# Kernel optimization log

Hardware: AMD Instinct MI355X
Metric: run time of the kernel (lower is better)

Reference implementation:

```python
import jax, jax.numpy as jnp
import numpy as np

N, E = 50000, 800000
IN, HID, HEADS, OUT = 128, 32, 8, 40
D1 = HID * HEADS  # 256


def setup_inputs() -> dict:
    key = jax.random.key(0)
    ks = jax.random.split(key, 24)

    def w(k, fin, fout):
        return (jax.random.normal(k, (fin, fout), jnp.float32) / np.sqrt(fin)).astype(jnp.float32)

    def b(k, fout):
        return (jax.random.normal(k, (fout,), jnp.float32) * 0.02).astype(jnp.float32)

    inp = {
        "x": jax.random.normal(ks[0], (N, IN), jnp.float32),
        "edge_index": jax.random.randint(ks[1], (2, E), 0, N, dtype=jnp.int64),
        # layer 1: TransformerConv(IN -> HID, heads=HEADS, concat=True, beta=True)
        "q1w": w(ks[2], IN, D1), "q1b": b(ks[3], D1),
        "k1w": w(ks[4], IN, D1), "k1b": b(ks[5], D1),
        "v1w": w(ks[6], IN, D1), "v1b": b(ks[7], D1),
        "s1w": w(ks[8], IN, D1), "s1b": b(ks[9], D1),
        "b1w": w(ks[10], 3 * D1, 1),
        # layer 2: TransformerConv(D1 -> OUT, heads=1, concat=False, beta=True)
        "q2w": w(ks[11], D1, OUT), "q2b": b(ks[12], OUT),
        "k2w": w(ks[13], D1, OUT), "k2b": b(ks[14], OUT),
        "v2w": w(ks[15], D1, OUT), "v2b": b(ks[16], OUT),
        "s2w": w(ks[17], D1, OUT), "s2b": b(ks[18], OUT),
        "b2w": w(ks[19], 3 * OUT, 1),
    }
    return inp


def _tconv(x, src, dst, qw, qb, kw, kb, vw, vb, sw, sb, bw, heads, ch, concat):
    """PyG TransformerConv (no edge_attr, root_weight=True, beta=True), eval mode."""
    n = x.shape[0]
    q = (x @ qw + qb).reshape(n, heads, ch)
    k = (x @ kw + kb).reshape(n, heads, ch)
    v = (x @ vw + vb).reshape(n, heads, ch)
    # per-edge attention logits: message flows src(j) -> dst(i)
    alpha = jnp.einsum("ehc,ehc->eh", q[dst], k[src]) / np.sqrt(ch)  # [E,H]
    # segment softmax over incoming edges of each dst node
    amax = jax.ops.segment_max(alpha, dst, num_segments=n)  # [N,H]
    a = jnp.exp(alpha - amax[dst])
    asum = jax.ops.segment_sum(a, dst, num_segments=n)  # [N,H]
    attn = a / asum[dst]  # [E,H]
    # scatter-aggregate weighted values
    out = jax.ops.segment_sum(v[src] * attn[:, :, None], dst, num_segments=n)  # [N,H,C]
    out = out.reshape(n, heads * ch) if concat else out.mean(axis=1)
    skip = x @ sw + sb
    beta = jax.nn.sigmoid(jnp.concatenate([out, skip, out - skip], axis=-1) @ bw)  # [N,1]
    return beta * skip + (1.0 - beta) * out


def reference(x, edge_index, q1w, q1b, k1w, k1b, v1w, v1b, s1w, s1b, b1w,
              q2w, q2b, k2w, k2b, v2w, v2b, s2w, s2b, b2w):
    src, dst = edge_index[0], edge_index[1]
    h = jax.nn.elu(_tconv(x, src, dst, q1w, q1b, k1w, k1b, v1w, v1b, s1w, s1b, b1w, HEADS, HID, True))
    return _tconv(h, src, dst, q2w, q2b, k2w, k2b, v2w, v2b, s2w, s2b, b2w, 1, OUT, False)
```

## Files before the change

### kernel.cpp

```cpp
#include <hip/hip_runtime.h>
#include <cstdint>
#include <cstddef>

#define N_NODES 50000
#define N_EDGES 800000
#define IN_F    128
#define HID     32
#define HEADS   8
#define OUT_F   40
#define D1      256
#define W1COLS  1024
#define W2COLS  160
#define CAP     64

#define GFILL_B   3125
#define G1_BX     391
#define G1_BY     8
#define G1_GEMM_B (G1_BX * G1_BY)
#define G1_TOTAL  (GFILL_B + G1_GEMM_B)

typedef unsigned short ushortT;
typedef unsigned char  ucharT;
typedef unsigned short ushortx8 __attribute__((ext_vector_type(8)));
typedef __bf16 bf16x8 __attribute__((ext_vector_type(8)));
typedef float floatx4 __attribute__((ext_vector_type(4)));
typedef float floatx2 __attribute__((ext_vector_type(2)));

__device__ inline ushortT f2bf(float f) {
    union { float f; unsigned int u; } c; c.f = f;
    unsigned int r = c.u + 0x7FFFu + ((c.u >> 16) & 1u);
    return (ushortT)(r >> 16);
}
__device__ inline float bf2f(ushortT h) {
    union { unsigned int u; float f; } c; c.u = ((unsigned int)h) << 16; return c.f;
}

#define PREP_Z_B     196
#define PREP_CONV_B  6250
#define PREP_W1_B    512
#define PREP_W2_B    160
#define PREP_TOTAL_B (PREP_Z_B + PREP_CONV_B + PREP_W1_B + PREP_W2_B)

__global__ __launch_bounds__(256) void k_prep(
        int* __restrict__ cursor,
        const float* __restrict__ x, ushortT* __restrict__ xb,
        const float* __restrict__ q1w, const float* __restrict__ k1w,
        const float* __restrict__ v1w, const float* __restrict__ s1w,
        const float* __restrict__ q1b, const float* __restrict__ k1b,
        const float* __restrict__ v1b, const float* __restrict__ s1b,
        ushortT* __restrict__ W1T, float* __restrict__ b1c,
        const float* __restrict__ q2w, const float* __restrict__ k2w,
        const float* __restrict__ v2w, const float* __restrict__ s2w,
        const float* __restrict__ q2b, const float* __restrict__ k2b,
        const float* __restrict__ v2b, const float* __restrict__ s2b,
        ushortT* __restrict__ W2T, float* __restrict__ b2c) {
    int b = blockIdx.x;
    int tid = threadIdx.x;
    if (b < PREP_Z_B) {
        int i = b * 256 + tid;
        if (i < N_NODES) cursor[i] = 0;
    } else if (b < PREP_Z_B + PREP_CONV_B) {
        int i = (b - PREP_Z_B) * 256 + tid;
        float4 v = reinterpret_cast<const float4*>(x)[i];
        ushort4 o;
        o.x = f2bf(v.x); o.y = f2bf(v.y); o.z = f2bf(v.z); o.w = f2bf(v.w);
        reinterpret_cast<ushort4*>(xb)[i] = o;
    } else if (b < PREP_Z_B + PREP_CONV_B + PREP_W1_B) {
        int t = (b - PREP_Z_B - PREP_CONV_B) * 256 + tid;
        int c = t / IN_F, k = t % IN_F;
        int sel = c >> 8, cc = c & 255;
        const float* w = sel == 0 ? q1w : sel == 1 ? k1w : sel == 2 ? v1w : s1w;
        W1T[(size_t)c * IN_F + k] = f2bf(w[(size_t)k * D1 + cc]);
        if (k == 0) {
            const float* bb = sel == 0 ? q1b : sel == 1 ? k1b : sel == 2 ? v1b : s1b;
            b1c[c] = bb[cc];
        }
    } else {
        int t = (b - PREP_Z_B - PREP_CONV_B - PREP_W1_B) * 256 + tid;
        int c = t / D1, k = t % D1;
        int sel = c / OUT_F, cc = c % OUT_F;
        const float* w = sel == 0 ? q2w : sel == 1 ? k2w : sel == 2 ? v2w : s2w;
        W2T[(size_t)c * D1 + k] = f2bf(w[(size_t)k * OUT_F + cc]);
        if (k == 0) {
            const float* bb = sel == 0 ? q2b : sel == 1 ? k2b : sel == 2 ? v2b : s2b;
            b2c[c] = bb[cc];
        }
    }
}

template<int MODE>
__global__ __launch_bounds__(256) void gemm_mfma_pack(
        const ushortT* __restrict__ A, const ushortT* __restrict__ BT,
        const float* __restrict__ bias, float* __restrict__ QSf,
        ushortT* __restrict__ QSh, ucharT* __restrict__ KV8,
        ushortT* __restrict__ K2V2,
        const int* __restrict__ ei, int* __restrict__ cursor, int* __restrict__ col,
        int M, int K, int Nn) {
    constexpr int TM = 128, TN = 128, TK = 32, LDP = 40;
    __shared__ ushortT smem[TM * LDP + TN * LDP];
    ushortT* As = smem;
    ushortT* Bs = smem + TM * LDP;
    int bx2, by2;
    if (MODE == 1) {
        int t = blockIdx.x;
        int idx;
        bool isFill;
        if (t < 2 * GFILL_B) { isFill = !(t & 1); idx = t >> 1; }
        else                 { isFill = false;    idx = t - GFILL_B; }
        if (isFill) {
            int e = idx * 256 + threadIdx.x;
            if (e < N_EDGES) {
                int dd = ei[N_EDGES + e];
                int p = atomicAdd(&cursor[dd], 1);
                col[dd * CAP + p] = ei[e];
            }
            return;
        }
        bx2 = idx % G1_BX;
        by2 = idx / G1_BX;
    } else {
        bx2 = blockIdx.x;
        by2 = blockIdx.y;
    }
    int tid = threadIdx.x;
    int lane = tid & 63, wave = tid >> 6;
    int bm = bx2 * TM, bn = by2 * TN;
    int wm = (wave & 1) * 64, wn = (wave >> 1) * 64;
    int mrow = lane & 15, g = lane >> 4;
    floatx4 acc[4][4] = {};

    for (int k0 = 0; k0 < K; k0 += TK) {
#pragma unroll
        for (int it = 0; it < 2; ++it) {
            int idx = tid + it * 256;
            int r = idx >> 2, c = (idx & 3) * 8;
            int gm = bm + r;
            ushortx8 val;
            if (gm < M) val = *reinterpret_cast<const ushortx8*>(A + (size_t)gm * K + k0 + c);
            else        val = (ushortx8)0;
            *reinterpret_cast<ushortx8*>(As + r * LDP + c) = val;
        }
#pragma unroll
        for (int it = 0; it < 2; ++it) {
            int idx = tid + it * 256;
            int r = idx >> 2, c = (idx & 3) * 8;
            int gn = bn + r;
            ushortx8 val;
            if (gn < Nn) val = *reinterpret_cast<const ushortx8*>(BT + (size_t)gn * K + k0 + c);
            else         val = (ushortx8)0;
            *reinterpret_cast<ushortx8*>(Bs + r * LDP + c) = val;
        }
        __syncthreads();
        {
            bf16x8 a[4], b[4];
#pragma unroll
            for (int i = 0; i < 4; ++i)
                a[i] = *reinterpret_cast<const bf16x8*>(As + (wm + i * 16 + mrow) * LDP + g * 8);
#pragma unroll
            for (int j = 0; j < 4; ++j)
                b[j] = *reinterpret_cast<const bf16x8*>(Bs + (wn + j * 16 + mrow) * LDP + g * 8);
#pragma unroll
            for (int i = 0; i < 4; ++i)
#pragma unroll
                for (int j = 0; j < 4; ++j)
                    acc[i][j] = __builtin_amdgcn_mfma_f32_16x16x32_bf16(a[i], b[j], acc[i][j], 0, 0, 0);
        }
        __syncthreads();
    }

    if (MODE == 1) {
        float* lds = reinterpret_cast<float*>(smem) + wave * 1088;
        int sec = by2 >> 1;
        int ccbase = (by2 & 1) * 128 + wn;
        int cb4 = (lane & 15) * 4;
        int rlo = lane >> 4;
        float4 bv = *reinterpret_cast<const float4*>(bias + by2 * 128 + wn + cb4);
#pragma unroll
        for (int i = 0; i < 4; ++i) {
#pragma unroll
            for (int j = 0; j < 4; ++j)
#pragma unroll
                for (int r = 0; r < 4; ++r)
                    lds[(g * 4 + r) * 68 + j * 16 + mrow] = acc[i][j][r];
#pragma unroll
            for (int it = 0; it < 4; ++it) {
                int row = it * 4 + rlo;
                int gm = bm + wm + i * 16 + row;
                if (gm >= M) continue;
                float4 v = *reinterpret_cast<float4*>(lds + row * 68 + cb4);
                v.x += bv.x; v.y += bv.y; v.z += bv.z; v.w += bv.w;
                int cc = ccbase + cb4;
                if (sec == 0 || sec == 3) {
                    ushort4 h;
                    h.x = f2bf(v.x); h.y = f2bf(v.y); h.z = f2bf(v.z); h.w = f2bf(v.w);
                    ushortT* dst = QSh + (size_t)gm * 512 + (sec == 3 ? 256 : 0) + cc;
                    *reinterpret_cast<ushort4*>(dst) = h;
                } else {
                    unsigned int pk = 0;
                    pk = __builtin_amdgcn_cvt_pk_fp8_f32(v.x, v.y, pk, false);
                    pk = __builtin_amdgcn_cvt_pk_fp8_f32(v.z, v.w, pk, true);
                    ucharT* dst = KV8 + (size_t)gm * 512 + (sec == 2 ? 256 : 0) + cc;
                    *reinterpret_cast<unsigned int*>(dst) = pk;
                }
            }
        }
    } else {
#pragma unroll
        for (int i = 0; i < 4; ++i) {
#pragma unroll
            for (int j = 0; j < 4; ++j) {
                int gn = bn + wn + j * 16 + mrow;
                if (gn >= Nn) continue;
                float bvs = bias[gn];
#pragma unroll
                for (int r = 0; r < 4; ++r) {
                    int gm = bm + wm + i * 16 + g * 4 + r;
                    if (gm >= M) continue;
                    float val = acc[i][j][r] + bvs;
                    int sec = gn / OUT_F, cc = gn % OUT_F;
                    if (sec == 0)      QSf[(size_t)gm * 80 + cc] = val;
                    else if (sec == 1) K2V2[(size_t)gm * 80 + cc] = f2bf(val);
                    else if (sec == 2) K2V2[(size_t)gm * 80 + 40 + cc] = f2bf(val);
                    else               QSf[(size_t)gm * 80 + 40 + cc] = val;
                }
            }
        }
    }
}

__global__ __launch_bounds__(256) void k_edge1(
        const ushortT* __restrict__ QSh, const ucharT* __restrict__ KV8,
        const float* __restrict__ bw,
        const int* __restrict__ degc, const int* __restrict__ col,
        ushortT* __restrict__ H1b) {
    int gid  = blockIdx.x * blockDim.x + threadIdx.x;
    int node = gid >> 6;
    int lane = threadIdx.x & 63;
    if (node >= N_NODES) return;
    const float scale = 0.17677669529663687f;
    ushort4 qh = *reinterpret_cast<const ushort4*>(QSh + (size_t)node * 512 + lane * 4);
    float4 q;
    q.x = bf2f(qh.x) * scale; q.y = bf2f(qh.y) * scale;
    q.z = bf2f(qh.z) * scale; q.w = bf2f(qh.w) * scale;

    float l = 0.f;
    float4 acc = make_float4(0.f, 0.f, 0.f, 0.f);
    int start = node * CAP;
    int d = degc[node];
    int t = 0;
    for (; t + 2 <= d; t += 2) {
        int j0 = col[start + t];
        int j1 = col[start + t + 1];
        const ucharT* row0 = KV8 + (size_t)j0 * 512 + lane * 4;
        const ucharT* row1 = KV8 + (size_t)j1 * 512 + lane * 4;
        unsigned int ku0 = *reinterpret_cast<const unsigned int*>(row0);
        unsigned int vu0 = *reinterpret_cast<const unsigned int*>(row0 + 256);
        unsigned int ku1 = *reinterpret_cast<const unsigned int*>(row1);
        unsigned int vu1 = *reinterpret_cast<const unsigned int*>(row1 + 256);
        floatx2 k0a = __builtin_amdgcn_cvt_pk_f32_fp8(ku0, false);
        floatx2 k0b = __builtin_amdgcn_cvt_pk_f32_fp8(ku0, true);
        floatx2 k1a = __builtin_amdgcn_cvt_pk_f32_fp8(ku1, false);
        floatx2 k1b = __builtin_amdgcn_cvt_pk_f32_fp8(ku1, true);
        float p0 = q.x * k0a[0] + q.y * k0a[1] + q.z * k0b[0] + q.w * k0b[1];
        float p1 = q.x * k1a[0] + q.y * k1a[1] + q.z * k1b[0] + q.w * k1b[1];
        p0 += __shfl_xor(p0, 1);  p1 += __shfl_xor(p1, 1);
        p0 += __shfl_xor(p0, 2);  p1 += __shfl_xor(p1, 2);
        p0 += __shfl_xor(p0, 4);  p1 += __shfl_xor(p1, 4);
        float e0 = __expf(p0);
        float e1 = __expf(p1);
        l += e0 + e1;
        floatx2 v0a = __builtin_amdgcn_cvt_pk_f32_fp8(vu0, false);
        floatx2 v0b = __builtin_amdgcn_cvt_pk_f32_fp8(vu0, true);
        floatx2 v1a = __builtin_amdgcn_cvt_pk_f32_fp8(vu1, false);
        floatx2 v1b = __builtin_amdgcn_cvt_pk_f32_fp8(vu1, true);
        acc.x += e0 * v0a[0] + e1 * v1a[0];
        acc.y += e0 * v0a[1] + e1 * v1a[1];
        acc.z += e0 * v0b[0] + e1 * v1b[0];
        acc.w += e0 * v0b[1] + e1 * v1b[1];
    }
    if (t < d) {
        int j = col[start + t];
        const ucharT* row = KV8 + (size_t)j * 512 + lane * 4;
        unsigned int ku = *reinterpret_cast<const unsigned int*>(row);
        unsigned int vu = *reinterpret_cast<const unsigned int*>(row + 256);
        floatx2 ka = __builtin_amdgcn_cvt_pk_f32_fp8(ku, false);
        floatx2 kb = __builtin_amdgcn_cvt_pk_f32_fp8(ku, true);
        float p0 = q.x * ka[0] + q.y * ka[1] + q.z * kb[0] + q.w * kb[1];
        p0 += __shfl_xor(p0, 1);
        p0 += __shfl_xor(p0, 2);
        p0 += __shfl_xor(p0, 4);
        float e0 = __expf(p0);
        l += e0;
        floatx2 va = __builtin_amdgcn_cvt_pk_f32_fp8(vu, false);
        floatx2 vb = __builtin_amdgcn_cvt_pk_f32_fp8(vu, true);
        acc.x += e0 * va[0];
        acc.y += e0 * va[1];
        acc.z += e0 * vb[0];
        acc.w += e0 * vb[1];
    }
    float inv = (l > 0.f) ? 1.f / l : 0.f;
    float4 o = make_float4(acc.x * inv, acc.y * inv, acc.z * inv, acc.w * inv);
    ushort4 sh = *reinterpret_cast<const ushort4*>(QSh + (size_t)node * 512 + 256 + lane * 4);
    float4 sk;
    sk.x = bf2f(sh.x); sk.y = bf2f(sh.y); sk.z = bf2f(sh.z); sk.w = bf2f(sh.w);
    const int c4 = lane * 4;
    float4 w0 = *reinterpret_cast<const float4*>(bw + c4);
    float4 w1 = *reinterpret_cast<const float4*>(bw + D1 + c4);
    float4 w2 = *reinterpret_cast<const float4*>(bw + 2 * D1 + c4);
    float part = o.x * w0.x + o.y * w0.y + o.z * w0.z + o.w * w0.w
               + sk.x * w1.x + sk.y * w1.y + sk.z * w1.z + sk.w * w1.w
               + (o.x - sk.x) * w2.x + (o.y - sk.y) * w2.y
               + (o.z - sk.z) * w2.z + (o.w - sk.w) * w2.w;
#pragma unroll
    for (int s = 1; s < 64; s <<= 1) part += __shfl_xor(part, s);
    float beta = 1.f / (1.f + __expf(-part));
    float4 h;
    h.x = beta * sk.x + (1.f - beta) * o.x;
    h.y = beta * sk.y + (1.f - beta) * o.y;
    h.z = beta * sk.z + (1.f - beta) * o.z;
    h.w = beta * sk.w + (1.f - beta) * o.w;
    h.x = h.x > 0.f ? h.x : __expf(h.x) - 1.f;
    h.y = h.y > 0.f ? h.y : __expf(h.y) - 1.f;
    h.z = h.z > 0.f ? h.z : __expf(h.z) - 1.f;
    h.w = h.w > 0.f ? h.w : __expf(h.w) - 1.f;
    ushort4 hb;
    hb.x = f2bf(h.x); hb.y = f2bf(h.y); hb.z = f2bf(h.z); hb.w = f2bf(h.w);
    *reinterpret_cast<ushort4*>(H1b + (size_t)node * D1 + c4) = hb;
}

__global__ __launch_bounds__(256) void k_edge2(
        const float* __restrict__ QS, const ushortT* __restrict__ K2V2,
        const float* __restrict__ bw,
        const int* __restrict__ degc, const int* __restrict__ col,
        float* __restrict__ out) {
    __shared__ float        qbuf[4][40];
    __shared__ float        attn[4][64];
    __shared__ int          jb[4][64];
    __shared__ unsigned int ksm[4][64 * 21];
    int gid  = blockIdx.x * blockDim.x + threadIdx.x;
    int node = gid >> 6;
    int wave = threadIdx.x >> 6;
    int lane = threadIdx.x & 63;
    if (node >= N_NODES) return;
    const float scale = 0.15811388300841897f;
    bool act = lane < OUT_F;
    if (act) qbuf[wave][lane] = QS[(size_t)node * 80 + lane] * scale;

    int d = degc[node];
    if (lane < d) jb[wave][lane] = col[node * CAP + lane];

    const unsigned int* Kdw = reinterpret_cast<const unsigned int*>(K2V2);
    int sr = lane / 20;
    int sc = lane - sr * 20;
    for (int r0 = 0; r0 < d; r0 += 3) {
        int rr = r0 + sr;
        if (lane < 60 && rr < d)
            ksm[wave][rr * 21 + sc] = Kdw[(size_t)jb[wave][rr] * 40 + sc];
    }

    float p = 0.f;
    if (lane < d) {
        float s = 0.f;
#pragma unroll
        for (int c = 0; c < 20; ++c) {
            unsigned int kk = ksm[wave][lane * 21 + c];
            s += qbuf[wave][2 * c]     * bf2f((ushortT)(kk & 0xFFFFu))
               + qbuf[wave][2 * c + 1] * bf2f((ushortT)(kk >> 16));
        }
        p = __expf(s);
    }
    attn[wave][lane] = p;
    float l = p;
#pragma unroll
    for (int s = 1; s < 64; s <<= 1) l += __shfl_xor(l, s);

    float acc = 0.f;
    int ln = act ? lane : 0;
    int e = 0;
    for (; e + 4 <= d; e += 4) {
        int je0 = jb[wave][e],     je1 = jb[wave][e + 1];
        int je2 = jb[wave][e + 2], je3 = jb[wave][e + 3];
        float v0 = bf2f(K2V2[(size_t)je0 * 80 + 40 + ln]);
        float v1 = bf2f(K2V2[(size_t)je1 * 80 + 40 + ln]);
        float v2 = bf2f(K2V2[(size_t)je2 * 80 + 40 + ln]);
        float v3 = bf2f(K2V2[(size_t)je3 * 80 + 40 + ln]);
        acc += (attn[wave][e] * v0 + attn[wave][e + 1] * v1)
             + (attn[wave][e + 2] * v2 + attn[wave][e + 3] * v3);
    }
    for (; e < d; ++e)
        acc += attn[wave][e] * bf2f(K2V2[(size_t)jb[wave][e] * 80 + 40 + ln]);

    float inv = (l > 0.f) ? 1.f / l : 0.f;
    float o  = acc * inv;
    float sk = act ? QS[(size_t)node * 80 + 40 + lane] : 0.f;
    float part = act ? (o * bw[lane] + sk * bw[OUT_F + lane] + (o - sk) * bw[2 * OUT_F + lane]) : 0.f;
#pragma unroll
    for (int s = 1; s < 64; s <<= 1) part += __shfl_xor(part, s);
    float beta = 1.f / (1.f + __expf(-part));
    if (act) out[(size_t)node * OUT_F + lane] = beta * sk + (1.f - beta) * o;
}

extern "C" void kernel_launch(void* const* d_in, const int* in_sizes, int n_in,
                              void* d_out, int out_size, void* d_ws, size_t ws_size,
                              hipStream_t stream) {
    const float* x   = (const float*)d_in[0];
    const int*   ei  = (const int*)d_in[1];
    const float* q1w = (const float*)d_in[2];
    const float* q1b = (const float*)d_in[3];
    const float* k1w = (const float*)d_in[4];
    const float* k1b = (const float*)d_in[5];
    const float* v1w = (const float*)d_in[6];
    const float* v1b = (const float*)d_in[7];
    const float* s1w = (const float*)d_in[8];
    const float* s1b = (const float*)d_in[9];
    const float* b1w = (const float*)d_in[10];
    const float* q2w = (const float*)d_in[11];
    const float* q2b = (const float*)d_in[12];
    const float* k2w = (const float*)d_in[13];
    const float* k2b = (const float*)d_in[14];
    const float* v2w = (const float*)d_in[15];
    const float* v2b = (const float*)d_in[16];
    const float* s2w = (const float*)d_in[17];
    const float* s2b = (const float*)d_in[18];
    const float* b2w = (const float*)d_in[19];
    float* out = (float*)d_out;

    char* w = (char*)d_ws;
    ushortT* QSh = (ushortT*)w;
    ucharT*  KV8 = (ucharT*)(w + 51200000);
    ushortT* H1b = (ushortT*)(w + 102400000);
    ushortT* xb  = (ushortT*)(w + 128000000);
    ushortT* W1T = (ushortT*)(w + 140800000);
    ushortT* W2T = (ushortT*)(w + 141062144);
    float*   b1c = (float*)(w + 141144064);
    float*   b2c = (float*)(w + 141148160);
    int* cursor  = (int*)(w + 141149184);
    int* col     = cursor + N_NODES;
    float*   QS2  = (float*)w;
    ushortT* K2V2 = (ushortT*)(w + 51200000);

    k_prep<<<PREP_TOTAL_B, 256, 0, stream>>>(
        cursor, x, xb,
        q1w, k1w, v1w, s1w, q1b, k1b, v1b, s1b, W1T, b1c,
        q2w, k2w, v2w, s2w, q2b, k2b, v2b, s2b, W2T, b2c);

    gemm_mfma_pack<1><<<G1_TOTAL, 256, 0, stream>>>(
        xb, W1T, b1c, nullptr, QSh, KV8, nullptr,
        ei, cursor, col, N_NODES, IN_F, W1COLS);

    k_edge1<<<(N_NODES * 64) / 256, 256, 0, stream>>>(QSh, KV8, b1w, cursor, col, H1b);

    dim3 g2((N_NODES + 127) / 128, (W2COLS + 127) / 128);
    gemm_mfma_pack<2><<<g2, 256, 0, stream>>>(H1b, W2T, b2c, QS2, nullptr, nullptr,
                                              K2V2, nullptr, nullptr, nullptr,
                                              N_NODES, D1, W2COLS);

    k_edge2<<<(N_NODES * 64) / 256, 256, 0, stream>>>(QS2, K2V2, b2w, cursor, col, out);
}
```

Measured before the change: 357.3 us.

## Fuse x fp32-to-bf16 conversion into first GEMM tile load; pack edge math

Removes the separate pass in the prep kernel that converted x to bf16. The first GEMM now loads fp32 x directly and rounds it to bf16 while staging its A tile, which saves a 25.6MB write and its later reread. In exchange, each of the 8 column-block groups re-reads and re-converts the fp32 rows, so the GEMM reads twice as many A bytes per tile. The edge kernels also rewrite their dot products and accumulations with 2-wide float vectors to encourage packed FMA instructions.

Measured after the change: 366.3 us. 2.5% more time.

```diff
diff --git a/kernel.cpp b/kernel.cpp
--- a/kernel.cpp
+++ b/kernel.cpp
@@ -36,14 +36,12 @@
 }
 
 #define PREP_Z_B     196
-#define PREP_CONV_B  6250
 #define PREP_W1_B    512
 #define PREP_W2_B    160
-#define PREP_TOTAL_B (PREP_Z_B + PREP_CONV_B + PREP_W1_B + PREP_W2_B)
+#define PREP_TOTAL_B (PREP_Z_B + PREP_W1_B + PREP_W2_B)
 
 __global__ __launch_bounds__(256) void k_prep(
         int* __restrict__ cursor,
-        const float* __restrict__ x, ushortT* __restrict__ xb,
         const float* __restrict__ q1w, const float* __restrict__ k1w,
         const float* __restrict__ v1w, const float* __restrict__ s1w,
         const float* __restrict__ q1b, const float* __restrict__ k1b,
@@ -59,14 +57,8 @@
     if (b < PREP_Z_B) {
         int i = b * 256 + tid;
         if (i < N_NODES) cursor[i] = 0;
-    } else if (b < PREP_Z_B + PREP_CONV_B) {
-        int i = (b - PREP_Z_B) * 256 + tid;
-        float4 v = reinterpret_cast<const float4*>(x)[i];
-        ushort4 o;
-        o.x = f2bf(v.x); o.y = f2bf(v.y); o.z = f2bf(v.z); o.w = f2bf(v.w);
-        reinterpret_cast<ushort4*>(xb)[i] = o;
-    } else if (b < PREP_Z_B + PREP_CONV_B + PREP_W1_B) {
-        int t = (b - PREP_Z_B - PREP_CONV_B) * 256 + tid;
+    } else if (b < PREP_Z_B + PREP_W1_B) {
+        int t = (b - PREP_Z_B) * 256 + tid;
         int c = t / IN_F, k = t % IN_F;
         int sel = c >> 8, cc = c & 255;
         const float* w = sel == 0 ? q1w : sel == 1 ? k1w : sel == 2 ? v1w : s1w;
@@ -76,7 +68,7 @@
             b1c[c] = bb[cc];
         }
     } else {
-        int t = (b - PREP_Z_B - PREP_CONV_B - PREP_W1_B) * 256 + tid;
+        int t = (b - PREP_Z_B - PREP_W1_B) * 256 + tid;
         int c = t / D1, k = t % D1;
         int sel = c / OUT_F, cc = c % OUT_F;
         const float* w = sel == 0 ? q2w : sel == 1 ? k2w : sel == 2 ? v2w : s2w;
@@ -90,7 +82,7 @@
 
 template<int MODE>
 __global__ __launch_bounds__(256) void gemm_mfma_pack(
-        const ushortT* __restrict__ A, const ushortT* __restrict__ BT,
+        const void* __restrict__ Ap, const ushortT* __restrict__ BT,
         const float* __restrict__ bias, float* __restrict__ QSf,
         ushortT* __restrict__ QSh, ucharT* __restrict__ KV8,
         ushortT* __restrict__ K2V2,
@@ -136,8 +128,19 @@
             int r = idx >> 2, c = (idx & 3) * 8;
             int gm = bm + r;
             ushortx8 val;
-            if (gm < M) val = *reinterpret_cast<const ushortx8*>(A + (size_t)gm * K + k0 + c);
-            else        val = (ushortx8)0;
+            if (MODE == 1) {
+                const float* Af = (const float*)Ap;
+                if (gm < M) {
+                    float4 a0 = *reinterpret_cast<const float4*>(Af + (size_t)gm * K + k0 + c);
+                    float4 a1 = *reinterpret_cast<const float4*>(Af + (size_t)gm * K + k0 + c + 4);
+                    val[0] = f2bf(a0.x); val[1] = f2bf(a0.y); val[2] = f2bf(a0.z); val[3] = f2bf(a0.w);
+                    val[4] = f2bf(a1.x); val[5] = f2bf(a1.y); val[6] = f2bf(a1.z); val[7] = f2bf(a1.w);
+                } else val = (ushortx8)0;
+            } else {
+                const ushortT* Ah = (const ushortT*)Ap;
+                if (gm < M) val = *reinterpret_cast<const ushortx8*>(Ah + (size_t)gm * K + k0 + c);
+                else        val = (ushortx8)0;
+            }
             *reinterpret_cast<ushortx8*>(As + r * LDP + c) = val;
         }
 #pragma unroll
@@ -239,12 +242,12 @@
     if (node >= N_NODES) return;
     const float scale = 0.17677669529663687f;
     ushort4 qh = *reinterpret_cast<const ushort4*>(QSh + (size_t)node * 512 + lane * 4);
-    float4 q;
-    q.x = bf2f(qh.x) * scale; q.y = bf2f(qh.y) * scale;
-    q.z = bf2f(qh.z) * scale; q.w = bf2f(qh.w) * scale;
+    floatx2 q01, q23;
+    q01[0] = bf2f(qh.x) * scale; q01[1] = bf2f(qh.y) * scale;
+    q23[0] = bf2f(qh.z) * scale; q23[1] = bf2f(qh.w) * scale;
 
     float l = 0.f;
-    float4 acc = make_float4(0.f, 0.f, 0.f, 0.f);
+    floatx2 acc01 = {0.f, 0.f}, acc23 = {0.f, 0.f};
     int start = node * CAP;
     int d = degc[node];
     int t = 0;
@@ -257,49 +260,43 @@
         unsigned int vu0 = *reinterpret_cast<const unsigned int*>(row0 + 256);
         unsigned int ku1 = *reinterpret_cast<const unsigned int*>(row1);
         unsigned int vu1 = *reinterpret_cast<const unsigned int*>(row1 + 256);
-        floatx2 k0a = __builtin_amdgcn_cvt_pk_f32_fp8(ku0, false);
-        floatx2 k0b = __builtin_amdgcn_cvt_pk_f32_fp8(ku0, true);
-        floatx2 k1a = __builtin_amdgcn_cvt_pk_f32_fp8(ku1, false);
-        floatx2 k1b = __builtin_amdgcn_cvt_pk_f32_fp8(ku1, true);
-        float p0 = q.x * k0a[0] + q.y * k0a[1] + q.z * k0b[0] + q.w * k0b[1];
-        float p1 = q.x * k1a[0] + q.y * k1a[1] + q.z * k1b[0] + q.w * k1b[1];
+        floatx2 t0 = q01 * __builtin_amdgcn_cvt_pk_f32_fp8(ku0, false)
+                   + q23 * __builtin_amdgcn_cvt_pk_f32_fp8(ku0, true);
+        floatx2 t1 = q01 * __builtin_amdgcn_cvt_pk_f32_fp8(ku1, false)
+                   + q23 * __builtin_amdgcn_cvt_pk_f32_fp8(ku1, true);
+        float p0 = t0[0] + t0[1];
+        float p1 = t1[0] + t1[1];
         p0 += __shfl_xor(p0, 1);  p1 += __shfl_xor(p1, 1);
         p0 += __shfl_xor(p0, 2);  p1 += __shfl_xor(p1, 2);
         p0 += __shfl_xor(p0, 4);  p1 += __shfl_xor(p1, 4);
         float e0 = __expf(p0);
         float e1 = __expf(p1);
         l += e0 + e1;
-        floatx2 v0a = __builtin_amdgcn_cvt_pk_f32_fp8(vu0, false);
-        floatx2 v0b = __builtin_amdgcn_cvt_pk_f32_fp8(vu0, true);
-        floatx2 v1a = __builtin_amdgcn_cvt_pk_f32_fp8(vu1, false);
-        floatx2 v1b = __builtin_amdgcn_cvt_pk_f32_fp8(vu1, true);
-        acc.x += e0 * v0a[0] + e1 * v1a[0];
-        acc.y += e0 * v0a[1] + e1 * v1a[1];
-        acc.z += e0 * v0b[0] + e1 * v1b[0];
-        acc.w += e0 * v0b[1] + e1 * v1b[1];
+        acc01 = acc01 + __builtin_amdgcn_cvt_pk_f32_fp8(vu0, false) * e0
+                      + __builtin_amdgcn_cvt_pk_f32_fp8(vu1, false) * e1;
+        acc23 = acc23 + __builtin_amdgcn_cvt_pk_f32_fp8(vu0, true) * e0
+                      + __builtin_amdgcn_cvt_pk_f32_fp8(vu1, true) * e1;
     }
     if (t < d) {
         int j = col[start + t];
         const ucharT* row = KV8 + (size_t)j * 512 + lane * 4;
         unsigned int ku = *reinterpret_cast<const unsigned int*>(row);
         unsigned int vu = *reinterpret_cast<const unsigned int*>(row + 256);
-        floatx2 ka = __builtin_amdgcn_cvt_pk_f32_fp8(ku, false);
-        floatx2 kb = __builtin_amdgcn_cvt_pk_f32_fp8(ku, true);
-        float p0 = q.x * ka[0] + q.y * ka[1] + q.z * kb[0] + q.w * kb[1];
+        floatx2 t0 = q01 * __builtin_amdgcn_cvt_pk_f32_fp8(ku, false)
+                   + q23 * __builtin_amdgcn_cvt_pk_f32_fp8(ku, true);
+        float p0 = t0[0] + t0[1];
         p0 += __shfl_xor(p0, 1);
         p0 += __shfl_xor(p0, 2);
         p0 += __shfl_xor(p0, 4);
         float e0 = __expf(p0);
         l += e0;
-        floatx2 va = __builtin_amdgcn_cvt_pk_f32_fp8(vu, false);
-        floatx2 vb = __builtin_amdgcn_cvt_pk_f32_fp8(vu, true);
-        acc.x += e0 * va[0];
-        acc.y += e0 * va[1];
-        acc.z += e0 * vb[0];
-        acc.w += e0 * vb[1];
+        acc01 = acc01 + __builtin_amdgcn_cvt_pk_f32_fp8(vu, false) * e0;
+        acc23 = acc23 + __builtin_amdgcn_cvt_pk_f32_fp8(vu, true) * e0;
     }
     float inv = (l > 0.f) ? 1.f / l : 0.f;
-    float4 o = make_float4(acc.x * inv, acc.y * inv, acc.z * inv, acc.w * inv);
+    float4 o;
+    o.x = acc01[0] * inv; o.y = acc01[1] * inv;
+    o.z = acc23[0] * inv; o.w = acc23[1] * inv;
     ushort4 sh = *reinterpret_cast<const ushort4*>(QSh + (size_t)node * 512 + 256 + lane * 4);
     float4 sk;
     sk.x = bf2f(sh.x); sk.y = bf2f(sh.y); sk.z = bf2f(sh.z); sk.w = bf2f(sh.w);
@@ -360,14 +357,15 @@
 
     float p = 0.f;
     if (lane < d) {
-        float s = 0.f;
+        floatx2 s2 = {0.f, 0.f};
 #pragma unroll
         for (int c = 0; c < 20; ++c) {
             unsigned int kk = ksm[wave][lane * 21 + c];
-            s += qbuf[wave][2 * c]     * bf2f((ushortT)(kk & 0xFFFFu))
-               + qbuf[wave][2 * c + 1] * bf2f((ushortT)(kk >> 16));
-        }
-        p = __expf(s);
+            floatx2 k2 = { bf2f((ushortT)(kk & 0xFFFFu)), bf2f((ushortT)(kk >> 16)) };
+            floatx2 q2 = { qbuf[wave][2 * c], qbuf[wave][2 * c + 1] };
+            s2 = s2 + q2 * k2;
+        }
+        p = __expf(s2[0] + s2[1]);
     }
     attn[wave][lane] = p;
     float l = p;
@@ -429,7 +427,6 @@
     ushortT* QSh = (ushortT*)w;
     ucharT*  KV8 = (ucharT*)(w + 51200000);
     ushortT* H1b = (ushortT*)(w + 102400000);
-    ushortT* xb  = (ushortT*)(w + 128000000);
     ushortT* W1T = (ushortT*)(w + 140800000);
     ushortT* W2T = (ushortT*)(w + 141062144);
     float*   b1c = (float*)(w + 141144064);
@@ -440,12 +437,12 @@
     ushortT* K2V2 = (ushortT*)(w + 51200000);
 
     k_prep<<<PREP_TOTAL_B, 256, 0, stream>>>(
-        cursor, x, xb,
+        cursor,
         q1w, k1w, v1w, s1w, q1b, k1b, v1b, s1b, W1T, b1c,
         q2w, k2w, v2w, s2w, q2b, k2b, v2b, s2b, W2T, b2c);
 
     gemm_mfma_pack<1><<<G1_TOTAL, 256, 0, stream>>>(
-        xb, W1T, b1c, nullptr, QSh, KV8, nullptr,
+        x, W1T, b1c, nullptr, QSh, KV8, nullptr,
         ei, cursor, col, N_NODES, IN_F, W1COLS);
 
     k_edge1<<<(N_NODES * 64) / 256, 256, 0, stream>>>(QSh, KV8, b1w, cursor, col, H1b);
```
